# Kernel tuning notes

Hardware: AMD Instinct MI355X
Metric: run time of the kernel (lower is better)

Reference implementation:

```python
import jax, jax.numpy as jnp
import numpy as np

N, M, E, D = 20000, 1024, 640000, 256


def setup_inputs() -> dict:
    key = jax.random.key(0)
    ks = jax.random.split(key, 24)
    mask = jax.random.uniform(ks[0], (N, M)) < 0.05
    init = jnp.where(mask, jax.random.uniform(ks[1], (N, M), minval=0.1, maxval=1.0), 0.0)
    inp = {
        'init': init,
        'ei_cc': jax.random.randint(ks[2], (2, E), 0, N, dtype=jnp.int32),
        'ei_cac': jax.random.randint(ks[3], (2, E), 0, N, dtype=jnp.int32),
        'ei_csc': jax.random.randint(ks[4], (2, E), 0, N, dtype=jnp.int32),
        'ea_cc': jax.random.uniform(ks[5], (E,), minval=0.1, maxval=1.0),
        'ea_cac': jax.random.uniform(ks[6], (E,), minval=0.1, maxval=1.0),
        'ea_csc': jax.random.uniform(ks[7], (E,), minval=0.1, maxval=1.0),
        # Projection MLP: Linear(1,16) -> ReLU -> Linear(16,D)
        'pW1': jax.random.normal(ks[8], (1, 16)) * 0.5,
        'pb1': jnp.zeros((16,)),
        'pW2': jax.random.normal(ks[9], (16, D)) * 0.1,
        'pb2': jnp.zeros((D,)),
        # three GCN branches, 3 layers each (all D->D)
        'W_cc': jax.random.normal(ks[10], (3, D, D)) * 0.05,
        'b_cc': jnp.zeros((3, D)),
        'W_cac': jax.random.normal(ks[11], (3, D, D)) * 0.05,
        'b_cac': jnp.zeros((3, D)),
        'W_csc': jax.random.normal(ks[12], (3, D, D)) * 0.05,
        'b_csc': jnp.zeros((3, D)),
        # meta-path attention: Linear(D, 1)
        'w_att': jax.random.normal(ks[13], (D,)) * 0.05,
        'b_att': jnp.zeros((1,)),
    }
    return inp


def projection(init, pW1, pb1, pW2, pb2):
    # torch code feeds the *indices* of nonzero columns through the MLP and
    # mean-pools per row. Vectorize: precompute MLP(j) for every column index j,
    # then masked mean.
    idx = jnp.arange(M, dtype=init.dtype)[:, None]          # [M, 1]
    h = jax.nn.relu(idx @ pW1 + pb1)                        # [M, 16]
    col_emb = h @ pW2 + pb2                                 # [M, D]
    mask = (init != 0).astype(init.dtype)                   # [N, M]
    cnt = mask.sum(axis=1)                                  # [N]
    emb = (mask @ col_emb) / jnp.maximum(cnt, 1.0)[:, None]
    return jnp.where(cnt[:, None] > 0, emb, 0.0)            # zero rows stay zero


def gcn_conv(x, edge_index, edge_weight, W, b):
    # PyG GCNConv with edge_weight: add self loops (w=1), symmetric norm.
    n = x.shape[0]
    loop = jnp.arange(n, dtype=edge_index.dtype)
    row = jnp.concatenate([edge_index[0], loop])
    col = jnp.concatenate([edge_index[1], loop])
    w = jnp.concatenate([edge_weight, jnp.ones((n,), x.dtype)])
    deg = jax.ops.segment_sum(w, col, num_segments=n)
    dinv = jnp.where(deg > 0, jax.lax.rsqrt(deg), 0.0)
    norm = dinv[row] * w * dinv[col]                        # [E+N]
    h = x @ W                                               # [N, D]
    out = jax.ops.segment_sum(norm[:, None] * h[row], col, num_segments=n)
    return out + b


def gcn_branch(x, edge_index, edge_weight, Ws, bs):
    for l in range(3):
        x = jax.nn.relu(gcn_conv(x, edge_index, edge_weight, Ws[l], bs[l]))
    return x


def reference(init, ei_cc, ei_cac, ei_csc, ea_cc, ea_cac, ea_csc,
              pW1, pb1, pW2, pb2, W_cc, b_cc, W_cac, b_cac, W_csc, b_csc,
              w_att, b_att):
    x0 = projection(init, pW1, pb1, pW2, pb2)               # [N, D]
    out_cc = gcn_branch(x0, ei_cc, ea_cc, W_cc, b_cc)
    out_cac = gcn_branch(x0, ei_cac, ea_cac, W_cac, b_cac)
    out_csc = gcn_branch(x0, ei_csc, ea_csc, W_csc, b_csc)
    emb = jnp.stack([out_cc, out_cac, out_csc], axis=0)     # [3, N, D]
    scores = jnp.einsum('pnd,d->pn', emb, w_att) + b_att[0] # [3, N]
    attn = jax.nn.softmax(scores, axis=0)                   # softmax over meta-paths
    return jnp.einsum('pn,pnd->nd', attn, emb)              # [N, D]
```

## Files before the change

kernel.cpp:

```cpp
#include <hip/hip_runtime.h>
#include <hip/hip_bf16.h>

typedef __hip_bfloat16 bf16;
typedef __bf16 v8bf __attribute__((ext_vector_type(8)));
typedef float f32x4 __attribute__((ext_vector_type(4)));

constexpr int N = 20000, M = 1024, E = 640000, D = 256;
constexpr size_t SEGEL = (size_t)N * D;
constexpr int NCHUNK = 10000;
constexpr int NSLICE = 64;
constexpr int ESLICE = E / NSLICE;

__device__ __forceinline__ float b2f(bf16 v) { return __bfloat162float(v); }
__device__ __forceinline__ bf16 f2b(float f) { return __float2bfloat16(f); }
__device__ __forceinline__ float u2f(unsigned short u) { return __uint_as_float(((unsigned)u) << 16); }
__device__ __forceinline__ unsigned short f2u(float f) { bf16 h = __float2bfloat16(f); return *(unsigned short*)&h; }
__device__ __forceinline__ float loadf(const void* p, size_t i, int isbf) {
    return isbf ? b2f(((const bf16*)p)[i]) : ((const float*)p)[i];
}
__device__ __forceinline__ void fma8(float* acc, uint4 v, float w) {
    acc[0] = fmaf(w, u2f((unsigned short)(v.x & 0xffffu)), acc[0]);
    acc[1] = fmaf(w, u2f((unsigned short)(v.x >> 16)), acc[1]);
    acc[2] = fmaf(w, u2f((unsigned short)(v.y & 0xffffu)), acc[2]);
    acc[3] = fmaf(w, u2f((unsigned short)(v.y >> 16)), acc[3]);
    acc[4] = fmaf(w, u2f((unsigned short)(v.z & 0xffffu)), acc[4]);
    acc[5] = fmaf(w, u2f((unsigned short)(v.z >> 16)), acc[5]);
    acc[6] = fmaf(w, u2f((unsigned short)(v.w & 0xffffu)), acc[6]);
    acc[7] = fmaf(w, u2f((unsigned short)(v.w >> 16)), acc[7]);
}
__device__ __forceinline__ unsigned pack2(float a, float b) {
    return (unsigned)f2u(a) | ((unsigned)f2u(b) << 16);
}

__global__ void detect_kernel(const void* __restrict__ ea, int* __restrict__ flag)
{
    if (threadIdx.x == 0 && blockIdx.x == 0) {
        const unsigned short* u = (const unsigned short*)ea;
        int cnt = 0;
        for (int i = 0; i < 64; i++) {
            float f = __uint_as_float(((unsigned)u[i]) << 16);
            if (f >= 0.05f && f <= 1.05f) cnt++;
        }
        *flag = (cnt >= 60) ? 1 : 0;
    }
}

__global__ __launch_bounds__(256) void transpose_kernel(
    const void* __restrict__ W0, const void* __restrict__ W1, const void* __restrict__ W2,
    bf16* __restrict__ WT, const int* __restrict__ flag)
{
    int isbf = *flag;
    int b = blockIdx.x;
    int mat = b >> 8, n = b & 255, k = threadIdx.x;
    const void* W = (mat < 3) ? W0 : (mat < 6) ? W1 : W2;
    int lm = mat - (mat < 3 ? 0 : (mat < 6 ? 3 : 6));
    WT[(size_t)mat * 65536 + n * 256 + k] =
        f2b(loadf(W, (size_t)lm * 65536 + k * 256 + n, isbf));
}

__global__ __launch_bounds__(256) void col_embT_kernel(
    const void* __restrict__ pW1, const void* __restrict__ pb1,
    const void* __restrict__ pW2, const void* __restrict__ pb2,
    bf16* __restrict__ cembT, const int* __restrict__ flag)
{
    int isbf = *flag;
    int j = blockIdx.y * 256 + threadIdx.x;
    int d = blockIdx.x;
    float jf = (float)j;
    float acc = loadf(pb2, d, isbf);
    #pragma unroll
    for (int k = 0; k < 16; k++) {
        float h = fmaxf(jf * loadf(pW1, k, isbf) + loadf(pb1, k, isbf), 0.0f);
        acc += h * loadf(pW2, k * 256 + d, isbf);
    }
    cembT[(size_t)d * 1024 + j] = f2b(acc);
}

__global__ __launch_bounds__(256) void proj_gemm_kernel(
    const void* __restrict__ init, const bf16* __restrict__ cembT,
    bf16* __restrict__ x0, const int* __restrict__ flag)
{
    int isbf = *flag;
    int wave = threadIdx.x >> 6, lane = threadIdx.x & 63;
    int m0 = blockIdx.x * 32 + (wave >> 1) * 16;
    int n0 = (wave & 1) * 128;
    int mrow = lane & 15, q = lane >> 4;
    f32x4 acc[8] = {};
    float cnt = 0.0f;
    for (int k0 = 0; k0 < 1024; k0 += 32) {
        int kb = k0 + q * 8;
        v8bf a;
        if (isbf) {
            const unsigned short* ar = (const unsigned short*)init + (size_t)(m0 + mrow) * 1024 + kb;
            ushort4 lo = *(const ushort4*)ar;
            ushort4 hi = *(const ushort4*)(ar + 4);
            unsigned short wv[8] = {lo.x, lo.y, lo.z, lo.w, hi.x, hi.y, hi.z, hi.w};
            #pragma unroll
            for (int j = 0; j < 8; j++) {
                bool nz = (wv[j] & 0x7fffu) != 0;
                a[j] = nz ? (__bf16)1.0f : (__bf16)0.0f;
                cnt += nz ? 1.0f : 0.0f;
            }
        } else {
            const float* ar = (const float*)init + (size_t)(m0 + mrow) * 1024 + kb;
            float4 lo = *(const float4*)ar;
            float4 hi = *(const float4*)(ar + 4);
            float wv[8] = {lo.x, lo.y, lo.z, lo.w, hi.x, hi.y, hi.z, hi.w};
            #pragma unroll
            for (int j = 0; j < 8; j++) {
                bool nz = wv[j] != 0.0f;
                a[j] = nz ? (__bf16)1.0f : (__bf16)0.0f;
                cnt += nz ? 1.0f : 0.0f;
            }
        }
        #pragma unroll
        for (int nt = 0; nt < 8; nt++) {
            const v8bf* brow = (const v8bf*)(cembT + (size_t)(n0 + nt * 16 + mrow) * 1024);
            acc[nt] = __builtin_amdgcn_mfma_f32_16x16x32_bf16(a, brow[kb >> 3], acc[nt], 0, 0, 0);
        }
    }
    cnt += __shfl_xor(cnt, 16, 64);
    cnt += __shfl_xor(cnt, 32, 64);
    float rinv[4];
    #pragma unroll
    for (int r = 0; r < 4; r++) {
        float c = __shfl(cnt, q * 4 + r, 64);
        rinv[r] = 1.0f / fmaxf(c, 1.0f);
    }
    #pragma unroll
    for (int nt = 0; nt < 8; nt++) {
        int col = n0 + nt * 16 + mrow;
        #pragma unroll
        for (int r = 0; r < 4; r++) {
            int row = m0 + q * 4 + r;
            x0[(size_t)row * 256 + col] = f2b(acc[nt][r] * rinv[r]);
        }
    }
}

__global__ __launch_bounds__(256) void countP_kernel(
    const int* __restrict__ e0, const int* __restrict__ e1, const int* __restrict__ e2,
    int* __restrict__ P)
{
    __shared__ int cur[NCHUNK];
    int b = blockIdx.x;
    int pb = b >> 7, rem = b & 127;
    int ck = rem >> 6, s = rem & 63;
    const int* ei = pb == 0 ? e0 : pb == 1 ? e1 : e2;
    int c0 = ck * NCHUNK;
    int t = threadIdx.x;
    for (int i = t; i < NCHUNK; i += 256) cur[i] = 0;
    __syncthreads();
    int ebase = s * ESLICE;
    for (int e = ebase + t; e < ebase + ESLICE; e += 256) {
        int c = ei[E + e];
        if (c >= c0 && c < c0 + NCHUNK) atomicAdd(&cur[c - c0], 1);
    }
    __syncthreads();
    int* Prow = P + ((size_t)(pb * NSLICE + s)) * N + c0;
    for (int i = t; i < NCHUNK; i += 256) Prow[i] = cur[i];
}

__global__ __launch_bounds__(256) void cnt_sum_kernel(
    const int* __restrict__ P, int* __restrict__ cnt)
{
    int id = blockIdx.x * 256 + threadIdx.x;
    if (id >= 3 * N) return;
    int pb = id / N, c = id - pb * N;
    int sum = 0;
    #pragma unroll 8
    for (int s = 0; s < NSLICE; s++)
        sum += P[((size_t)(pb * NSLICE + s)) * N + c];
    cnt[id] = sum;
}

__global__ __launch_bounds__(1024) void scan_kernel(
    const int* __restrict__ cnt, int* __restrict__ col_ptr)
{
    int pb = blockIdx.x;
    int base = pb * E;
    __shared__ int s[1024];
    int t = threadIdx.x;
    const int CH = 20;
    int i0 = t * CH;
    int sum = 0;
    for (int j = 0; j < CH; j++) { int i = i0 + j; if (i < N) sum += cnt[pb * N + i]; }
    s[t] = sum;
    __syncthreads();
    for (int off = 1; off < 1024; off <<= 1) {
        int v = (t >= off) ? s[t - off] : 0;
        __syncthreads();
        s[t] += v;
        __syncthreads();
    }
    int run = base + s[t] - sum;
    for (int j = 0; j < CH; j++) {
        int i = i0 + j;
        if (i < N) {
            col_ptr[pb * (N + 1) + i] = run;
            run += cnt[pb * N + i];
        }
    }
    if (t == 0) col_ptr[pb * (N + 1) + N] = base + E;
}

__global__ __launch_bounds__(256) void base_kernel(
    int* __restrict__ P, const int* __restrict__ col_ptr)
{
    int id = blockIdx.x * 256 + threadIdx.x;
    if (id >= 3 * N) return;
    int pb = id / N, c = id - pb * N;
    int run = col_ptr[pb * (N + 1) + c];
    for (int s = 0; s < NSLICE; s++) {
        size_t idx = ((size_t)(pb * NSLICE + s)) * N + c;
        int v = P[idx];
        P[idx] = run;
        run += v;
    }
}

__global__ __launch_bounds__(256) void fill_kernel(
    const int* __restrict__ e0, const int* __restrict__ e1, const int* __restrict__ e2,
    const void* __restrict__ a0, const void* __restrict__ a1, const void* __restrict__ a2,
    const int* __restrict__ P, int* __restrict__ srow, float* __restrict__ swv,
    const int* __restrict__ flag)
{
    __shared__ int cur[NCHUNK];
    int isbf = *flag;
    int b = blockIdx.x;
    int pb = b >> 7, rem = b & 127;
    int ck = rem >> 6, s = rem & 63;
    const int* ei = pb == 0 ? e0 : pb == 1 ? e1 : e2;
    const void* ea = pb == 0 ? a0 : pb == 1 ? a1 : a2;
    int c0 = ck * NCHUNK;
    int t = threadIdx.x;
    const int* Prow = P + ((size_t)(pb * NSLICE + s)) * N + c0;
    for (int i = t; i < NCHUNK; i += 256) cur[i] = Prow[i];
    __syncthreads();
    int ebase = s * ESLICE;
    for (int e = ebase + t; e < ebase + ESLICE; e += 256) {
        int c = ei[E + e];
        if (c >= c0 && c < c0 + NCHUNK) {
            int r = ei[e];
            float w = loadf(ea, e, isbf);
            int pos = atomicAdd(&cur[c - c0], 1);
            srow[pos] = r;
            swv[pos] = w;
        }
    }
}

__global__ __launch_bounds__(256) void degsum_kernel(
    const int* __restrict__ col_ptr, const float* __restrict__ swv,
    float* __restrict__ dinv, float* __restrict__ nloop)
{
    int wave = threadIdx.x >> 6, lane = threadIdx.x & 63;
    int pb = blockIdx.x / 5000;
    int i = (blockIdx.x - pb * 5000) * 4 + wave;
    int start = col_ptr[pb * (N + 1) + i], end = col_ptr[pb * (N + 1) + i + 1];
    float sum = 0.0f;
    for (int p = start + lane; p < end; p += 64) sum += swv[p];
    for (int off = 1; off < 64; off <<= 1) sum += __shfl_xor(sum, off, 64);
    if (lane == 0) {
        float dg = 1.0f + sum;
        dinv[pb * N + i] = rsqrtf(dg);
        nloop[pb * N + i] = 1.0f / dg;
    }
}

__global__ __launch_bounds__(256) void snorm_kernel(
    const int* __restrict__ col_ptr, const int* __restrict__ srow,
    float* __restrict__ swv, const float* __restrict__ dinv)
{
    int wave = threadIdx.x >> 6, lane = threadIdx.x & 63;
    int pb = blockIdx.x / 5000;
    int i = (blockIdx.x - pb * 5000) * 4 + wave;
    int start = col_ptr[pb * (N + 1) + i], end = col_ptr[pb * (N + 1) + i + 1];
    float dc = dinv[pb * N + i];
    for (int p = start + lane; p < end; p += 64) {
        int r = srow[p];
        swv[p] = dc * swv[p] * dinv[pb * N + r];
    }
}

__global__ __launch_bounds__(256) void aggregate_kernel(
    const bf16* __restrict__ xi0, const bf16* __restrict__ xi1, const bf16* __restrict__ xi2,
    bf16* __restrict__ yb,
    const int* __restrict__ col_ptr, const int* __restrict__ srow,
    const float* __restrict__ snorm, const float* __restrict__ nloop)
{
    int wave = threadIdx.x >> 6, lane = threadIdx.x & 63;
    int pb = blockIdx.x / 5000;
    int i = (blockIdx.x - pb * 5000) * 4 + wave;
    const bf16* x = pb == 0 ? xi0 : pb == 1 ? xi1 : xi2;
    const uint4* xr = (const uint4*)x;
    int L = lane & 31, h = lane >> 5;
    int start = col_ptr[pb * (N + 1) + i], end = col_ptr[pb * (N + 1) + i + 1];
    float nl = nloop[pb * N + i];
    float acc[8];
    {
        uint4 sv = xr[(size_t)i * 32 + L];
        float self = (h == 0) ? nl : 0.0f;
        #pragma unroll
        for (int j = 0; j < 8; j++) acc[j] = 0.0f;
        fma8(acc, sv, self);
    }
    for (int base = start; base < end; base += 64) {
        int n = end - base; n = n < 64 ? n : 64;
        int r = 0; float w = 0.0f;
        if (lane < n) { r = srow[base + lane]; w = snorm[base + lane]; }
        #pragma unroll 4
        for (int jj = 0; jj < n; jj += 2) {
            int rj = __shfl(r, jj + h, 64);
            float wj = __shfl(w, jj + h, 64);
            uint4 v = xr[(size_t)rj * 32 + L];
            fma8(acc, v, wj);
        }
    }
    #pragma unroll
    for (int j = 0; j < 8; j++) acc[j] += __shfl_xor(acc[j], 32, 64);
    if (h == 0) {
        uint4 o;
        o.x = pack2(acc[0], acc[1]);
        o.y = pack2(acc[2], acc[3]);
        o.z = pack2(acc[4], acc[5]);
        o.w = pack2(acc[6], acc[7]);
        ((uint4*)yb)[(size_t)pb * (SEGEL / 8) + (size_t)i * 32 + L] = o;
    }
}

__global__ __launch_bounds__(256) void gemm_relu_kernel(
    const bf16* __restrict__ yb, const bf16* __restrict__ WT, int layer,
    const void* __restrict__ b0, const void* __restrict__ b1, const void* __restrict__ b2,
    bf16* __restrict__ o0, bf16* __restrict__ o1, bf16* __restrict__ o2,
    const int* __restrict__ flag)
{
    int isbf = *flag;
    int pl = blockIdx.x / 625, blk = blockIdx.x - pl * 625;
    const bf16* y = yb + (size_t)pl * SEGEL;
    const bf16* wt = WT + (size_t)(pl * 3 + layer) * 65536;
    const void* bias = pl == 0 ? b0 : pl == 1 ? b1 : b2;
    bf16* xout = pl == 0 ? o0 : pl == 1 ? o1 : o2;

    int wave = threadIdx.x >> 6, lane = threadIdx.x & 63;
    int m0 = blk * 32 + (wave >> 1) * 16;
    int n0 = (wave & 1) * 128;
    int mrow = lane & 15, q = lane >> 4;

    f32x4 acc[8] = {};
    const v8bf* arow = reinterpret_cast<const v8bf*>(y + (size_t)(m0 + mrow) * 256);
    for (int k0 = 0; k0 < 256; k0 += 32) {
        v8bf a = arow[(k0 >> 3) + q];
        #pragma unroll
        for (int nt = 0; nt < 8; nt++) {
            const v8bf* brow = reinterpret_cast<const v8bf*>(wt + (size_t)(n0 + nt * 16 + mrow) * 256);
            acc[nt] = __builtin_amdgcn_mfma_f32_16x16x32_bf16(a, brow[(k0 >> 3) + q], acc[nt], 0, 0, 0);
        }
    }
    #pragma unroll
    for (int nt = 0; nt < 8; nt++) {
        int col = n0 + nt * 16 + mrow;
        float bv = loadf(bias, (size_t)layer * 256 + col, isbf);
        #pragma unroll
        for (int r = 0; r < 4; r++) {
            int row = m0 + q * 4 + r;
            xout[(size_t)row * 256 + col] = f2b(fmaxf(acc[nt][r] + bv, 0.0f));
        }
    }
}

__global__ __launch_bounds__(256) void attention_kernel(
    const bf16* __restrict__ e0, const bf16* __restrict__ e1, const bf16* __restrict__ e2,
    const void* __restrict__ w_att, void* __restrict__ out, int n_nodes,
    const int* __restrict__ flag)
{
    int isbf = *flag;
    int wave = threadIdx.x >> 6, lane = threadIdx.x & 63;
    int n = blockIdx.x * 4 + wave;
    if (n >= n_nodes) return;
    int d0 = lane * 4;
    float w[4], v0[4], v1[4], v2[4];
    #pragma unroll
    for (int j = 0; j < 4; j++) {
        w[j]  = loadf(w_att, d0 + j, isbf);
        v0[j] = b2f(e0[(size_t)n * 256 + d0 + j]);
        v1[j] = b2f(e1[(size_t)n * 256 + d0 + j]);
        v2[j] = b2f(e2[(size_t)n * 256 + d0 + j]);
    }
    float s0 = 0, s1 = 0, s2 = 0;
    #pragma unroll
    for (int j = 0; j < 4; j++) { s0 += v0[j] * w[j]; s1 += v1[j] * w[j]; s2 += v2[j] * w[j]; }
    for (int off = 1; off < 64; off <<= 1) {
        s0 += __shfl_xor(s0, off, 64);
        s1 += __shfl_xor(s1, off, 64);
        s2 += __shfl_xor(s2, off, 64);
    }
    float m = fmaxf(s0, fmaxf(s1, s2));
    float a0 = expf(s0 - m), a1 = expf(s1 - m), a2 = expf(s2 - m);
    float inv = 1.0f / (a0 + a1 + a2);
    a0 *= inv; a1 *= inv; a2 *= inv;
    #pragma unroll
    for (int j = 0; j < 4; j++) {
        float v = a0 * v0[j] + a1 * v1[j] + a2 * v2[j];
        if (isbf) ((bf16*)out)[(size_t)n * 256 + d0 + j] = f2b(v);
        else      ((float*)out)[(size_t)n * 256 + d0 + j] = v;
    }
}

extern "C" void kernel_launch(void* const* d_in, const int* in_sizes, int n_in,
                              void* d_out, int out_size, void* d_ws, size_t ws_size,
                              hipStream_t stream)
{
    (void)in_sizes; (void)n_in; (void)out_size; (void)ws_size;

    const void* init = d_in[0];
    const int*  ei[3] = {(const int*)d_in[1], (const int*)d_in[2], (const int*)d_in[3]};
    const void* ea[3] = {d_in[4], d_in[5], d_in[6]};
    const void* pW1 = d_in[7];
    const void* pb1 = d_in[8];
    const void* pW2 = d_in[9];
    const void* pb2 = d_in[10];
    const void* Wb[3] = {d_in[11], d_in[13], d_in[15]};
    const void* bb[3] = {d_in[12], d_in[14], d_in[16]};
    const void* w_att = d_in[17];

    char* ws = (char*)d_ws;
    size_t off = 0;
    auto carve = [&](size_t bytes) -> char* {
        off = (off + 255) & ~(size_t)255;
        char* p = ws + off; off += bytes; return p;
    };
    int*   flag  = (int*)carve(4);
    bf16*  WT    = (bf16*)carve((size_t)9 * 65536 * 2);
    bf16*  cembT = (bf16*)carve((size_t)D * M * 2);
    bf16*  x0    = (bf16*)carve(SEGEL * 2);
    int*   cnt   = (int*)carve((size_t)3 * N * 4);
    int*   colp  = (int*)carve((size_t)3 * (N + 1) * 4);
    float* dinv  = (float*)carve((size_t)3 * N * 4);
    float* nloop = (float*)carve((size_t)3 * N * 4);
    int*   srow  = (int*)carve((size_t)3 * E * 4);
    float* swv   = (float*)carve((size_t)3 * E * 4);
    bf16*  ybuf  = (bf16*)carve((size_t)3 * SEGEL * 2);
    bf16*  bufA  = (bf16*)carve((size_t)3 * SEGEL * 2);
    bf16*  bufB  = (bf16*)carve((size_t)3 * SEGEL * 2);
    int* P = (int*)bufB;

    detect_kernel<<<1, 64, 0, stream>>>(ea[0], flag);
    transpose_kernel<<<2304, 256, 0, stream>>>(Wb[0], Wb[1], Wb[2], WT, flag);
    col_embT_kernel<<<dim3(256, 4), 256, 0, stream>>>(pW1, pb1, pW2, pb2, cembT, flag);
    proj_gemm_kernel<<<625, 256, 0, stream>>>(init, cembT, x0, flag);

    countP_kernel<<<384, 256, 0, stream>>>(ei[0], ei[1], ei[2], P);
    cnt_sum_kernel<<<(3 * N + 255) / 256, 256, 0, stream>>>(P, cnt);
    scan_kernel<<<3, 1024, 0, stream>>>(cnt, colp);
    base_kernel<<<(3 * N + 255) / 256, 256, 0, stream>>>(P, colp);
    fill_kernel<<<384, 256, 0, stream>>>(ei[0], ei[1], ei[2], ea[0], ea[1], ea[2],
                                         P, srow, swv, flag);
    degsum_kernel<<<15000, 256, 0, stream>>>(colp, swv, dinv, nloop);
    snorm_kernel<<<15000, 256, 0, stream>>>(colp, srow, swv, dinv);

    const bf16 *i0 = x0, *i1 = x0, *i2 = x0;
    bf16* dsts[3] = {bufA, bufB, bufA};
    for (int l = 0; l < 3; l++) {
        aggregate_kernel<<<15000, 256, 0, stream>>>(i0, i1, i2, ybuf, colp, srow, swv, nloop);
        bf16* dst = dsts[l];
        gemm_relu_kernel<<<1875, 256, 0, stream>>>(ybuf, WT, l, bb[0], bb[1], bb[2],
                                                   dst, dst + SEGEL, dst + 2 * SEGEL, flag);
        i0 = dst; i1 = dst + SEGEL; i2 = dst + 2 * SEGEL;
    }
    attention_kernel<<<5000, 256, 0, stream>>>(bufA, bufA + SEGEL, bufA + 2 * SEGEL,
                                               w_att, d_out, N, flag);
}
```

Before: 969.5 us.

## Pack edge row/weight into int2 and retile projection and GCN GEMMs for more blocks

Replaces the separate srow and swv arrays with one interleaved int2 array, so the fill, degree, normalisation and aggregation kernels each do one 8-byte access per edge instead of two 4-byte ones. The aggregate inner loop unroll rises from 4 to 8. The projection GEMM now has each block cover 16 rows by 128 columns, and the GCN GEMM splits N into two halves, which raises the block count to 2500 and 3750 and cuts per-wave accumulators. In exchange, A-tile loads and the init mask conversion are repeated across column blocks, and each wave gets less MFMA work per load.

```diff
diff --git a/kernel.cpp b/kernel.cpp
--- a/kernel.cpp
+++ b/kernel.cpp
@@ -82,10 +82,11 @@
 {
     int isbf = *flag;
     int wave = threadIdx.x >> 6, lane = threadIdx.x & 63;
-    int m0 = blockIdx.x * 32 + (wave >> 1) * 16;
-    int n0 = (wave & 1) * 128;
+    int mblk = blockIdx.x >> 1, nh = blockIdx.x & 1;
+    int m0 = mblk * 16;
+    int n0 = nh * 128 + wave * 32;
     int mrow = lane & 15, q = lane >> 4;
-    f32x4 acc[8] = {};
+    f32x4 acc[2] = {};
     float cnt = 0.0f;
     for (int k0 = 0; k0 < 1024; k0 += 32) {
         int kb = k0 + q * 8;
@@ -114,7 +115,7 @@
             }
         }
         #pragma unroll
-        for (int nt = 0; nt < 8; nt++) {
+        for (int nt = 0; nt < 2; nt++) {
             const v8bf* brow = (const v8bf*)(cembT + (size_t)(n0 + nt * 16 + mrow) * 1024);
             acc[nt] = __builtin_amdgcn_mfma_f32_16x16x32_bf16(a, brow[kb >> 3], acc[nt], 0, 0, 0);
         }
@@ -128,7 +129,7 @@
         rinv[r] = 1.0f / fmaxf(c, 1.0f);
     }
     #pragma unroll
-    for (int nt = 0; nt < 8; nt++) {
+    for (int nt = 0; nt < 2; nt++) {
         int col = n0 + nt * 16 + mrow;
         #pragma unroll
         for (int r = 0; r < 4; r++) {
@@ -222,8 +223,7 @@
 __global__ __launch_bounds__(256) void fill_kernel(
     const int* __restrict__ e0, const int* __restrict__ e1, const int* __restrict__ e2,
     const void* __restrict__ a0, const void* __restrict__ a1, const void* __restrict__ a2,
-    const int* __restrict__ P, int* __restrict__ srow, float* __restrict__ swv,
-    const int* __restrict__ flag)
+    const int* __restrict__ P, int2* __restrict__ epack, const int* __restrict__ flag)
 {
     __shared__ int cur[NCHUNK];
     int isbf = *flag;
@@ -244,14 +244,14 @@
             int r = ei[e];
             float w = loadf(ea, e, isbf);
             int pos = atomicAdd(&cur[c - c0], 1);
-            srow[pos] = r;
-            swv[pos] = w;
+            int2 v; v.x = r; v.y = __float_as_int(w);
+            epack[pos] = v;
         }
     }
 }
 
 __global__ __launch_bounds__(256) void degsum_kernel(
-    const int* __restrict__ col_ptr, const float* __restrict__ swv,
+    const int* __restrict__ col_ptr, const int2* __restrict__ epack,
     float* __restrict__ dinv, float* __restrict__ nloop)
 {
     int wave = threadIdx.x >> 6, lane = threadIdx.x & 63;
@@ -259,7 +259,7 @@
     int i = (blockIdx.x - pb * 5000) * 4 + wave;
     int start = col_ptr[pb * (N + 1) + i], end = col_ptr[pb * (N + 1) + i + 1];
     float sum = 0.0f;
-    for (int p = start + lane; p < end; p += 64) sum += swv[p];
+    for (int p = start + lane; p < end; p += 64) sum += __int_as_float(epack[p].y);
     for (int off = 1; off < 64; off <<= 1) sum += __shfl_xor(sum, off, 64);
     if (lane == 0) {
         float dg = 1.0f + sum;
@@ -269,8 +269,8 @@
 }
 
 __global__ __launch_bounds__(256) void snorm_kernel(
-    const int* __restrict__ col_ptr, const int* __restrict__ srow,
-    float* __restrict__ swv, const float* __restrict__ dinv)
+    const int* __restrict__ col_ptr, int2* __restrict__ epack,
+    const float* __restrict__ dinv)
 {
     int wave = threadIdx.x >> 6, lane = threadIdx.x & 63;
     int pb = blockIdx.x / 5000;
@@ -278,16 +278,16 @@
     int start = col_ptr[pb * (N + 1) + i], end = col_ptr[pb * (N + 1) + i + 1];
     float dc = dinv[pb * N + i];
     for (int p = start + lane; p < end; p += 64) {
-        int r = srow[p];
-        swv[p] = dc * swv[p] * dinv[pb * N + r];
+        int2 v = epack[p];
+        epack[p].y = __float_as_int(dc * __int_as_float(v.y) * dinv[pb * N + v.x]);
     }
 }
 
 __global__ __launch_bounds__(256) void aggregate_kernel(
     const bf16* __restrict__ xi0, const bf16* __restrict__ xi1, const bf16* __restrict__ xi2,
     bf16* __restrict__ yb,
-    const int* __restrict__ col_ptr, const int* __restrict__ srow,
-    const float* __restrict__ snorm, const float* __restrict__ nloop)
+    const int* __restrict__ col_ptr, const int2* __restrict__ epack,
+    const float* __restrict__ nloop)
 {
     int wave = threadIdx.x >> 6, lane = threadIdx.x & 63;
     int pb = blockIdx.x / 5000;
@@ -307,12 +307,12 @@
     }
     for (int base = start; base < end; base += 64) {
         int n = end - base; n = n < 64 ? n : 64;
-        int r = 0; float w = 0.0f;
-        if (lane < n) { r = srow[base + lane]; w = snorm[base + lane]; }
-        #pragma unroll 4
+        int2 ep; ep.x = 0; ep.y = 0;
+        if (lane < n) ep = epack[base + lane];
+        #pragma unroll 8
         for (int jj = 0; jj < n; jj += 2) {
-            int rj = __shfl(r, jj + h, 64);
-            float wj = __shfl(w, jj + h, 64);
+            int rj = __shfl(ep.x, jj + h, 64);
+            float wj = __int_as_float(__shfl(ep.y, jj + h, 64));
             uint4 v = xr[(size_t)rj * 32 + L];
             fma8(acc, v, wj);
         }
@@ -336,29 +336,31 @@
     const int* __restrict__ flag)
 {
     int isbf = *flag;
-    int pl = blockIdx.x / 625, blk = blockIdx.x - pl * 625;
+    int pl = blockIdx.x / 1250;
+    int rem = blockIdx.x - pl * 1250;
+    int mblk = rem >> 1, nh = rem & 1;
     const bf16* y = yb + (size_t)pl * SEGEL;
     const bf16* wt = WT + (size_t)(pl * 3 + layer) * 65536;
     const void* bias = pl == 0 ? b0 : pl == 1 ? b1 : b2;
     bf16* xout = pl == 0 ? o0 : pl == 1 ? o1 : o2;
 
     int wave = threadIdx.x >> 6, lane = threadIdx.x & 63;
-    int m0 = blk * 32 + (wave >> 1) * 16;
-    int n0 = (wave & 1) * 128;
+    int m0 = mblk * 32 + (wave >> 1) * 16;
+    int n0 = nh * 128 + (wave & 1) * 64;
     int mrow = lane & 15, q = lane >> 4;
 
-    f32x4 acc[8] = {};
+    f32x4 acc[4] = {};
     const v8bf* arow = reinterpret_cast<const v8bf*>(y + (size_t)(m0 + mrow) * 256);
     for (int k0 = 0; k0 < 256; k0 += 32) {
         v8bf a = arow[(k0 >> 3) + q];
         #pragma unroll
-        for (int nt = 0; nt < 8; nt++) {
+        for (int nt = 0; nt < 4; nt++) {
             const v8bf* brow = reinterpret_cast<const v8bf*>(wt + (size_t)(n0 + nt * 16 + mrow) * 256);
             acc[nt] = __builtin_amdgcn_mfma_f32_16x16x32_bf16(a, brow[(k0 >> 3) + q], acc[nt], 0, 0, 0);
         }
     }
     #pragma unroll
-    for (int nt = 0; nt < 8; nt++) {
+    for (int nt = 0; nt < 4; nt++) {
         int col = n0 + nt * 16 + mrow;
         float bv = loadf(bias, (size_t)layer * 256 + col, isbf);
         #pragma unroll
@@ -438,8 +440,7 @@
     int*   colp  = (int*)carve((size_t)3 * (N + 1) * 4);
     float* dinv  = (float*)carve((size_t)3 * N * 4);
     float* nloop = (float*)carve((size_t)3 * N * 4);
-    int*   srow  = (int*)carve((size_t)3 * E * 4);
-    float* swv   = (float*)carve((size_t)3 * E * 4);
+    int2*  epack = (int2*)carve((size_t)3 * E * 8);
     bf16*  ybuf  = (bf16*)carve((size_t)3 * SEGEL * 2);
     bf16*  bufA  = (bf16*)carve((size_t)3 * SEGEL * 2);
     bf16*  bufB  = (bf16*)carve((size_t)3 * SEGEL * 2);
@@ -448,23 +449,23 @@
     detect_kernel<<<1, 64, 0, stream>>>(ea[0], flag);
     transpose_kernel<<<2304, 256, 0, stream>>>(Wb[0], Wb[1], Wb[2], WT, flag);
     col_embT_kernel<<<dim3(256, 4), 256, 0, stream>>>(pW1, pb1, pW2, pb2, cembT, flag);
-    proj_gemm_kernel<<<625, 256, 0, stream>>>(init, cembT, x0, flag);
+    proj_gemm_kernel<<<2500, 256, 0, stream>>>(init, cembT, x0, flag);
 
     countP_kernel<<<384, 256, 0, stream>>>(ei[0], ei[1], ei[2], P);
     cnt_sum_kernel<<<(3 * N + 255) / 256, 256, 0, stream>>>(P, cnt);
     scan_kernel<<<3, 1024, 0, stream>>>(cnt, colp);
     base_kernel<<<(3 * N + 255) / 256, 256, 0, stream>>>(P, colp);
     fill_kernel<<<384, 256, 0, stream>>>(ei[0], ei[1], ei[2], ea[0], ea[1], ea[2],
-                                         P, srow, swv, flag);
-    degsum_kernel<<<15000, 256, 0, stream>>>(colp, swv, dinv, nloop);
-    snorm_kernel<<<15000, 256, 0, stream>>>(colp, srow, swv, dinv);
+                                         P, epack, flag);
+    degsum_kernel<<<15000, 256, 0, stream>>>(colp, epack, dinv, nloop);
+    snorm_kernel<<<15000, 256, 0, stream>>>(colp, epack, dinv);
 
     const bf16 *i0 = x0, *i1 = x0, *i2 = x0;
     bf16* dsts[3] = {bufA, bufB, bufA};
     for (int l = 0; l < 3; l++) {
-        aggregate_kernel<<<15000, 256, 0, stream>>>(i0, i1, i2, ybuf, colp, srow, swv, nloop);
+        aggregate_kernel<<<15000, 256, 0, stream>>>(i0, i1, i2, ybuf, colp, epack, nloop);
         bf16* dst = dsts[l];
-        gemm_relu_kernel<<<1875, 256, 0, stream>>>(ybuf, WT, l, bb[0], bb[1], bb[2],
+        gemm_relu_kernel<<<3750, 256, 0, stream>>>(ybuf, WT, l, bb[0], bb[1], bb[2],
                                                    dst, dst + SEGEL, dst + 2 * SEGEL, flag);
         i0 = dst; i1 = dst + SEGEL; i2 = dst + 2 * SEGEL;
     }
```

Result: slower. 1.008 ms (+4.0%).
